# Kernel tuning notes

Measured on AMD Instinct MI355X. Metric: run time of the kernel, lower is better.

Reference implementation:

```python
import jax, jax.numpy as jnp
import numpy as np

PH, CH, Z, H, W, NK = 4, 8, 8, 320, 320, 4096
ITERS, GAMMA, TAU, EPS, RATIO = 3, 0.1, 0.2, 0.01, 0.2
LO, HI = int(Z * RATIO), Z - int(Z * RATIO)  # effective_slice = slice(1, 7)
TWO_PI = 2.0 * np.pi


def to_c(x):
    return jax.lax.complex(x[..., 0], x[..., 1])


def warp(img, flow):
    # MVF motion warp. img: (PH, Z, H, W) complex; flow: (PH, 2, Z, H, W) pixel displacements.
    gy = jnp.clip(jnp.arange(H, dtype=flow.dtype)[:, None] + flow[:, 0], 0.0, H - 1.0)
    gx = jnp.clip(jnp.arange(W, dtype=flow.dtype)[None, :] + flow[:, 1], 0.0, W - 1.0)
    y0 = jnp.floor(gy); x0 = jnp.floor(gx)
    wy = gy - y0; wx = gx - x0
    y0 = y0.astype(jnp.int32); x0 = x0.astype(jnp.int32)
    y1 = jnp.minimum(y0 + 1, H - 1); x1 = jnp.minimum(x0 + 1, W - 1)
    flat = img.reshape(PH, Z, H * W)
    def g(yi, xi):
        return jnp.take_along_axis(flat, (yi * W + xi).reshape(PH, Z, H * W), axis=-1).reshape(PH, Z, H, W)
    return (g(y0, x0) * ((1 - wy) * (1 - wx)) + g(y0, x1) * ((1 - wy) * wx)
            + g(y1, x0) * (wy * (1 - wx)) + g(y1, x1) * (wy * wx))


def nufft(img, traj):
    # Type-2 NUFFT via FFT + bilinear k-space interpolation.
    # img: (PH, CH, Z, H, W) complex; traj: (PH, 2, NK) in [-pi, pi).
    F = jnp.fft.fftshift(jnp.fft.fft2(img), axes=(-2, -1))
    gy = jnp.clip((traj[:, 0] / TWO_PI + 0.5) * H, 0.0, H - 1.0)
    gx = jnp.clip((traj[:, 1] / TWO_PI + 0.5) * W, 0.0, W - 1.0)
    def samp(Fp, gyp, gxp):
        y0 = jnp.floor(gyp); x0 = jnp.floor(gxp)
        wy = gyp - y0; wx = gxp - x0
        y0 = y0.astype(jnp.int32); x0 = x0.astype(jnp.int32)
        y1 = jnp.minimum(y0 + 1, H - 1); x1 = jnp.minimum(x0 + 1, W - 1)
        return (Fp[..., y0, x0] * ((1 - wy) * (1 - wx)) + Fp[..., y0, x1] * ((1 - wy) * wx)
                + Fp[..., y1, x0] * (wy * (1 - wx)) + Fp[..., y1, x1] * (wy * wx))
    return jax.vmap(samp)(F, gy, gx)  # (PH, CH, Z, NK)


def forward_model(x, mvf, csm_c, traj):
    # A = NUFFT * CSM * MVF
    warped = warp(x, mvf)                # (PH, Z, H, W)
    coil = csm_c[None] * warped[:, None]  # (PH, CH, Z, H, W)
    return nufft(coil, traj)             # (PH, CH, Z, NK)


def tv_energy(x):
    # smooth (anisotropic) TV energy; grad_reg = std * d/dx TV(x) = x_eff - regularization(x_eff)
    dy = x[..., 1:, :] - x[..., :-1, :]
    dx = x[..., :, 1:] - x[..., :, :-1]
    return jnp.sum(jnp.sqrt(jnp.abs(dy) ** 2 + 1e-8)) + jnp.sum(jnp.sqrt(jnp.abs(dx) ** 2 + 1e-8))


def setup_inputs():
    key = jax.random.key(0)
    ks = jax.random.split(key, 6)
    kspace_data = 0.1 * jax.random.normal(ks[0], (1, PH, CH, Z, NK, 2), jnp.float32)
    kspace_traj = jax.random.uniform(ks[1], (PH, 2, NK), jnp.float32, -np.pi, np.pi)
    image_init = jax.random.normal(ks[2], (1, PH, Z, H, W, 2), jnp.float32)
    mvf = 2.0 * jax.random.normal(ks[3], (PH, 2, Z, H, W), jnp.float32)
    csm = jax.random.normal(ks[4], (CH, Z, H, W, 2), jnp.float32) / np.sqrt(CH)
    std = jax.random.uniform(ks[5], (1,), jnp.float32, 0.05, 0.15)
    return {"kspace_data": kspace_data, "kspace_traj": kspace_traj, "image_init": image_init,
            "mvf": mvf, "csm": csm, "std": std}


def reference(kspace_data, kspace_traj, image_init, mvf, csm, std):
    y = to_c(kspace_data)[0]                   # (PH, CH, Z, NK)
    x = to_c(jnp.nan_to_num(image_init))[0]     # (PH, Z, H, W)
    csm_c = to_c(csm)                           # (CH, Z, H, W)
    s = std[0]

    def dc_loss(xv):
        est = forward_model(xv, mvf, csm_c, kspace_traj)[:, :, LO:HI]
        det = jax.lax.stop_gradient(jnp.abs(est))
        w = 1.0 / (det / det.max() + EPS)
        d = w * (est - y[:, :, LO:HI])
        # MSE over view_as_real = mean of squared real components
        return 0.5 * (jnp.mean(d.real ** 2) + jnp.mean(d.imag ** 2))

    for _ in range(ITERS):
        g_dc = jax.grad(dc_loss)(x)
        g_tv = s * jax.grad(tv_energy)(x[:, LO:HI])
        g_reg = jnp.zeros_like(x).at[:, LO:HI].set(g_tv)
        x = x - (GAMMA * g_dc + TAU * g_reg)
    return jnp.stack([x.real, x.imag], axis=-1)[None]  # (1, PH, Z, H, W, 2)
```

## Files before the change

kernel.cpp:

```cpp
#include <hip/hip_runtime.h>
#include <math.h>

#define PH   4
#define CHN  8
#define ZT   8
#define ZE   6
#define HG   320
#define WG   320
#define HW2  102400
#define NKP  4096
#define LSTR 321
#define FBCAP 131072u

constexpr float GAMMA_C = 0.1f;
constexpr float TAU_C   = 0.2f;
constexpr float EPS_C   = 0.01f;
constexpr float INV_N   = 1.0f / 786432.0f;
#define TWO_PI_F 6.28318530717958647692f

constexpr float W5R[5] = { 1.f,  0.30901699f, -0.80901699f, -0.80901699f,  0.30901699f};
constexpr float W5I[5] = { 0.f, -0.95105652f, -0.58778525f,  0.58778525f,  0.95105652f};

__device__ __forceinline__ float2 cmul(float2 a, float2 b){
  return make_float2(a.x*b.x - a.y*b.y, a.x*b.y + a.y*b.x);
}
__device__ __forceinline__ void cmac(float2& d, float2 a, float2 b){
  d.x = fmaf(a.x, b.x, fmaf(-a.y, b.y, d.x));
  d.y = fmaf(a.x, b.y, fmaf( a.y, b.x, d.y));
}

__device__ __forceinline__ unsigned pk(float2 v){
  unsigned ua = __float_as_uint(v.x), ub = __float_as_uint(v.y);
  ua = (ua + 0x7FFFu + ((ua >> 16) & 1u)) >> 16;
  ub = (ub + 0x7FFFu + ((ub >> 16) & 1u)) >> 16;
  return ua | (ub << 16);
}
__device__ __forceinline__ float2 upk(unsigned v){
  return make_float2(__uint_as_float(v << 16), __uint_as_float(v & 0xFFFF0000u));
}

__device__ __forceinline__ void corners(float gy, float gx, int& y0, int& x0, int& y1, int& x1,
                                        float& w00, float& w01, float& w10, float& w11){
  float y0f = floorf(gy), x0f = floorf(gx);
  float wy = gy - y0f, wx = gx - x0f;
  y0 = (int)y0f; x0 = (int)x0f;
  y1 = min(y0 + 1, HG - 1); x1 = min(x0 + 1, WG - 1);
  w00 = (1.f - wy) * (1.f - wx);
  w01 = (1.f - wy) * wx;
  w10 = wy * (1.f - wx);
  w11 = wy * wx;
}

__device__ __forceinline__ void traj_to_grid(float ty, float tx, float& gy, float& gx){
  gy = fminf(fmaxf((ty / TWO_PI_F + 0.5f) * 320.f, 0.f), 319.f);
  gx = fminf(fmaxf((tx / TWO_PI_F + 0.5f) * 320.f, 0.f), 319.f);
}

struct FT {
  float2 t1, t2, t3, t4;
  float2 tw0, tw1, tw2, tw3, tw4;
  int br5, lane;
};

__device__ __forceinline__ FT ft_init(){
  FT f; int l = (int)(threadIdx.x & 63); f.lane = l;
  sincosf(-TWO_PI_F * (float)l * (1.0f/320.0f), &f.t1.y, &f.t1.x);
  f.t2 = cmul(f.t1, f.t1); f.t3 = cmul(f.t2, f.t1); f.t4 = cmul(f.t2, f.t2);
  sincosf(-TWO_PI_F * (float)(l & 31) * (1.0f/64.0f), &f.tw0.y, &f.tw0.x);
  sincosf(-TWO_PI_F * (float)(l & 15) * (1.0f/32.0f), &f.tw1.y, &f.tw1.x);
  sincosf(-TWO_PI_F * (float)(l &  7) * (1.0f/16.0f), &f.tw2.y, &f.tw2.x);
  sincosf(-TWO_PI_F * (float)(l &  3) * (1.0f/ 8.0f), &f.tw3.y, &f.tw3.x);
  f.tw4 = (l & 1) ? make_float2(0.f, -1.f) : make_float2(1.f, 0.f);
  int br = ((l&1)<<5) | ((l&2)<<3) | ((l&4)<<1) | ((l&8)>>1) | ((l&16)>>3) | ((l&32)>>5);
  f.br5 = 5 * br;
  return f;
}

template<int H>
__device__ __forceinline__ void bfly(float2& v, float2 tw, int lane){
  float px = __shfl_xor(v.x, H, 64);
  float py = __shfl_xor(v.y, H, 64);
  bool up = (lane & H) != 0;
  float ax = up ? px : v.x, ay = up ? py : v.y;
  float bx = up ? v.x : px, by = up ? v.y : py;
  float dx = ax - bx,  dy = ay - by;
  float mx = fmaf(dx, tw.x, -dy * tw.y);
  float my = fmaf(dx, tw.y,  dy * tw.x);
  v.x = up ? mx : (ax + bx);
  v.y = up ? my : (ay + by);
}

__device__ __forceinline__ void fft320w(const float2 a[5], const FT& f, float2* __restrict__ seg){
  float2 z[5];
  #pragma unroll
  for (int r = 0; r < 5; r++){
    float2 acc = a[0];
    #pragma unroll
    for (int q = 1; q < 5; q++){
      const int j = (q * r) % 5;
      cmac(acc, a[q], make_float2(W5R[j], W5I[j]));
    }
    z[r] = acc;
  }
  z[1] = cmul(z[1], f.t1); z[2] = cmul(z[2], f.t2);
  z[3] = cmul(z[3], f.t3); z[4] = cmul(z[4], f.t4);
  #pragma unroll
  for (int r = 0; r < 5; r++){
    float2 v = z[r];
    bfly<32>(v, f.tw0, f.lane);
    bfly<16>(v, f.tw1, f.lane);
    bfly< 8>(v, f.tw2, f.lane);
    bfly< 4>(v, f.tw3, f.lane);
    bfly< 2>(v, f.tw4, f.lane);
    {
      float px = __shfl_xor(v.x, 1, 64);
      float py = __shfl_xor(v.y, 1, 64);
      bool up = (f.lane & 1) != 0;
      float ax = up ? px : v.x, ay = up ? py : v.y;
      float bx = up ? v.x : px, by = up ? v.y : py;
      v.x = up ? (ax - bx) : (ax + bx);
      v.y = up ? (ay - by) : (ay + by);
    }
    seg[f.br5 + r] = v;
  }
}

__device__ __forceinline__ void fft320w_pk(const float2 a[5], const FT& f, unsigned* __restrict__ seg){
  float2 z[5];
  #pragma unroll
  for (int r = 0; r < 5; r++){
    float2 acc = a[0];
    #pragma unroll
    for (int q = 1; q < 5; q++){
      const int j = (q * r) % 5;
      cmac(acc, a[q], make_float2(W5R[j], W5I[j]));
    }
    z[r] = acc;
  }
  z[1] = cmul(z[1], f.t1); z[2] = cmul(z[2], f.t2);
  z[3] = cmul(z[3], f.t3); z[4] = cmul(z[4], f.t4);
  #pragma unroll
  for (int r = 0; r < 5; r++){
    float2 v = z[r];
    bfly<32>(v, f.tw0, f.lane);
    bfly<16>(v, f.tw1, f.lane);
    bfly< 8>(v, f.tw2, f.lane);
    bfly< 4>(v, f.tw3, f.lane);
    bfly< 2>(v, f.tw4, f.lane);
    {
      float px = __shfl_xor(v.x, 1, 64);
      float py = __shfl_xor(v.y, 1, 64);
      bool up = (f.lane & 1) != 0;
      float ax = up ? px : v.x, ay = up ? py : v.y;
      float bx = up ? v.x : px, by = up ? v.y : py;
      v.x = up ? (ax - bx) : (ax + bx);
      v.y = up ? (ay - by) : (ay + by);
    }
    seg[f.br5 + r] = pk(v);
  }
}

__global__ __launch_bounds__(256) void k_khist(const float* __restrict__ traj, unsigned* __restrict__ xhist){
  int gid = blockIdx.x * 256 + threadIdx.x;
  if (gid >= PH * NKP) return;
  int p = gid >> 12, k = gid & (NKP - 1);
  float gy, gx;
  traj_to_grid(traj[(p * 2 + 0) * NKP + k], traj[(p * 2 + 1) * NKP + k], gy, gx);
  atomicAdd(&xhist[p * WG + (int)floorf(gx)], 1u);
}

__global__ void k_kscan(const unsigned* __restrict__ xhist, unsigned* __restrict__ xcur,
                        unsigned* __restrict__ xbnd){
  int p = threadIdx.x;
  if (p < PH){
    unsigned acc = 0;
    for (int b = 0; b < WG; b++){ xcur[p * WG + b] = acc; xbnd[p * (WG + 1) + b] = acc; acc += xhist[p * WG + b]; }
    xbnd[p * (WG + 1) + WG] = acc;
  }
}

__global__ __launch_bounds__(256) void k_kperm(const float* __restrict__ traj, unsigned* __restrict__ xcur,
                                               float4* __restrict__ permx){
  int gid = blockIdx.x * 256 + threadIdx.x;
  if (gid >= PH * NKP) return;
  int p = gid >> 12, k = gid & (NKP - 1);
  float gy, gx;
  traj_to_grid(traj[(p * 2 + 0) * NKP + k], traj[(p * 2 + 1) * NKP + k], gy, gx);
  unsigned sx = atomicAdd(&xcur[p * WG + (int)floorf(gx)], 1u);
  permx[p * NKP + sx] = make_float4(__uint_as_float((unsigned)k), gy, gx, 0.f);
}

__global__ __launch_bounds__(256) void k_pack_csm(const float2* __restrict__ csm, unsigned* __restrict__ csmb, int n){
  int i = blockIdx.x * 256 + threadIdx.x;
  if (i < n) csmb[i] = pk(csm[i]);
}

__global__ __launch_bounds__(256) void k_init(const float2* __restrict__ img0, float2* __restrict__ x, int n){
  int i = blockIdx.x * 256 + threadIdx.x;
  if (i < n){
    float2 v = img0[i];
    v.x = isnan(v.x) ? 0.f : fminf(fmaxf(v.x, -3.4028235e38f), 3.4028235e38f);
    v.y = isnan(v.y) ? 0.f : fminf(fmaxf(v.y, -3.4028235e38f), 3.4028235e38f);
    x[i] = v;
  }
}

__global__ __launch_bounds__(256) void k_warp_tv(const float2* __restrict__ x, const float* __restrict__ mvf,
                                                 unsigned* __restrict__ warped, unsigned* __restrict__ gtv,
                                                 unsigned int* __restrict__ dmax, unsigned int* __restrict__ fbcnt){
  if (blockIdx.x == 0 && threadIdx.x == 0){ *dmax = 0u; *fbcnt = 0u; }
  int gid = blockIdx.x * 256 + threadIdx.x;
  int hw = gid % HW2;
  int pz = gid / HW2;
  int zz = pz % ZE, p = pz / ZE, z = zz + 1;
  int h = hw / WG, w = hw - h * WG;
  const float* mv = mvf + ((size_t)(p * 2 + 0) * ZT + z) * HW2;
  float fy = mv[hw];
  float fx = mv[(size_t)ZT * HW2 + hw];
  float gy = fminf(fmaxf((float)h + fy, 0.f), 319.f);
  float gx = fminf(fmaxf((float)w + fx, 0.f), 319.f);
  int y0, x0, y1, x1; float w00, w01, w10, w11;
  corners(gy, gx, y0, x0, y1, x1, w00, w01, w10, w11);
  const float2* xs = x + (size_t)(p * ZT + z) * HW2;
  float2 v00 = xs[y0 * WG + x0], v01 = xs[y0 * WG + x1];
  float2 v10 = xs[y1 * WG + x0], v11 = xs[y1 * WG + x1];
  float2 o;
  o.x = v00.x * w00 + v01.x * w01 + v10.x * w10 + v11.x * w11;
  o.y = v00.y * w00 + v01.y * w01 + v10.y * w10 + v11.y * w11;
  warped[gid] = pk(o);
  float2 xc = xs[hw];
  float tre = 0.f, tim = 0.f;
  if (h > 0){
    float2 n = xs[hw - WG];
    float dr = xc.x - n.x, di = xc.y - n.y;
    float r = sqrtf(dr * dr + di * di + 1e-8f);
    tre += dr / r; tim += di / r;
  }
  if (h < HG - 1){
    float2 n = xs[hw + WG];
    float dr = n.x - xc.x, di = n.y - xc.y;
    float r = sqrtf(dr * dr + di * di + 1e-8f);
    tre -= dr / r; tim -= di / r;
  }
  if (w > 0){
    float2 n = xs[hw - 1];
    float dr = xc.x - n.x, di = xc.y - n.y;
    float r = sqrtf(dr * dr + di * di + 1e-8f);
    tre += dr / r; tim += di / r;
  }
  if (w < WG - 1){
    float2 n = xs[hw + 1];
    float dr = n.x - xc.x, di = n.y - xc.y;
    float r = sqrtf(dr * dr + di * di + 1e-8f);
    tre -= dr / r; tim -= di / r;
  }
  gtv[gid] = pk(make_float2(tre, -tim));
}

__global__ __launch_bounds__(512) void k_fft_row_fwd(const unsigned* __restrict__ warped, const unsigned* __restrict__ csmb,
                                                     unsigned* __restrict__ FT_, int p0){
  __shared__ float2 seg[16 * LSTR];
  FT f = ft_init();
  int wid = threadIdx.x >> 6, l = f.lane;
  int hg = blockIdx.x % 20; int sl = blockIdx.x / 20;
  int zz = sl % ZE; int s2 = sl / ZE; int c = s2 % CHN; int pp = s2 / CHN;
  int p = p0 + pp; int z = zz + 1;
  int h0 = hg * 16 + wid * 2;
  const unsigned* wr0 = warped + ((size_t)(p * ZE + zz)) * HW2 + (size_t)h0 * WG;
  const unsigned* cs0 = csmb + ((size_t)(c * ZT + z)) * HW2 + (size_t)h0 * WG;
  float sgn0 = ((h0 + l) & 1) ? -1.f : 1.f;
  float2 a0[5], a1[5];
  #pragma unroll
  for (int q = 0; q < 5; q++){
    float2 v0 = cmul(upk(wr0[64 * q + l]), upk(cs0[64 * q + l]));
    float2 v1 = cmul(upk(wr0[WG + 64 * q + l]), upk(cs0[WG + 64 * q + l]));
    a0[q] = make_float2(v0.x * sgn0, v0.y * sgn0);
    a1[q] = make_float2(-v1.x * sgn0, -v1.y * sgn0);
  }
  fft320w(a0, f, seg + (wid * 2) * LSTR);
  fft320w(a1, f, seg + (wid * 2 + 1) * LSTR);
  __syncthreads();
  unsigned* out = FT_ + (size_t)sl * HW2 + hg * 16;
  for (int i = threadIdx.x; i < 16 * WG; i += 512){
    int w = i >> 4; int hh = i & 15;
    out[(size_t)w * HG + hh] = pk(seg[hh * LSTR + w]);
  }
}

__global__ __launch_bounds__(256) void k_fft_col_sample(const unsigned* __restrict__ FT_, const float4* __restrict__ permx,
                                                        const unsigned* __restrict__ xbnd, float2* __restrict__ est,
                                                        unsigned int* __restrict__ dmax, int p0){
  __shared__ unsigned seg[2][9 * LSTR];
  FT f = ft_init();
  int tid = threadIdx.x; int wid = tid >> 6, l = f.lane;
  int cg = blockIdx.x % 40; int pr = blockIdx.x / 40;
  int sl0 = pr * 2;
  int s2 = sl0 / ZE; int pp = s2 / CHN;
  int p = p0 + pp;
  int cbase = cg * 8;
  const int ncol = (cbase + 8 <= WG - 1) ? 9 : 8;
  const unsigned* Fs0 = FT_ + (size_t)sl0 * HW2 + (size_t)cbase * HG;
  const unsigned* Fs1 = Fs0 + HW2;
  unsigned raw0[3][5], raw1[3][5];
  #pragma unroll
  for (int cc = 0; cc < 3; cc++){
    int col = cc * 4 + wid;
    if (col < 9){
      int colc = min(col, ncol - 1);
      const unsigned* s0 = Fs0 + (size_t)colc * HG;
      const unsigned* s1 = Fs1 + (size_t)colc * HG;
      #pragma unroll
      for (int q = 0; q < 5; q++){ raw0[cc][q] = s0[64 * q + l]; raw1[cc][q] = s1[64 * q + l]; }
    }
  }
  #pragma unroll
  for (int cc = 0; cc < 3; cc++){
    int col = cc * 4 + wid;
    if (col < 9){
      int colc = min(col, ncol - 1);
      float2 a0[5], a1[5];
      #pragma unroll
      for (int q = 0; q < 5; q++){ a0[q] = upk(raw0[cc][q]); a1[q] = upk(raw1[cc][q]); }
      fft320w_pk(a0, f, seg[0] + colc * LSTR);
      fft320w_pk(a1, f, seg[1] + colc * LSTR);
    }
  }
  __syncthreads();
  int lo = (int)xbnd[p * (WG + 1) + cbase];
  int hi = (int)xbnd[p * (WG + 1) + min(cbase + 8, WG)];
  float2* eb0 = est + ((size_t)(p0 * CHN * ZE) + sl0) * NKP;
  float2* eb1 = eb0 + NKP;
  const float4* px = permx + p * NKP;
  float md2 = 0.f;
  for (int j = lo + tid; j < hi; j += 256){
    float4 e4 = px[j];
    int y0, x0, y1, x1; float w00, w01, w10, w11;
    corners(e4.y, e4.z, y0, x0, y1, x1, w00, w01, w10, w11);
    int lc0 = x0 - cbase, lc1 = x1 - cbase;
    {
      float2 v00 = upk(seg[0][lc0 * LSTR + y0]), v01 = upk(seg[0][lc1 * LSTR + y0]);
      float2 v10 = upk(seg[0][lc0 * LSTR + y1]), v11 = upk(seg[0][lc1 * LSTR + y1]);
      float2 e;
      e.x = v00.x * w00 + v01.x * w01 + v10.x * w10 + v11.x * w11;
      e.y = v00.y * w00 + v01.y * w01 + v10.y * w10 + v11.y * w11;
      eb0[j] = e;
      md2 = fmaxf(md2, e.x * e.x + e.y * e.y);
    }
    {
      float2 v00 = upk(seg[1][lc0 * LSTR + y0]), v01 = upk(seg[1][lc1 * LSTR + y0]);
      float2 v10 = upk(seg[1][lc0 * LSTR + y1]), v11 = upk(seg[1][lc1 * LSTR + y1]);
      float2 e;
      e.x = v00.x * w00 + v01.x * w01 + v10.x * w10 + v11.x * w11;
      e.y = v00.y * w00 + v01.y * w01 + v10.y * w10 + v11.y * w11;
      eb1[j] = e;
      md2 = fmaxf(md2, e.x * e.x + e.y * e.y);
    }
  }
  for (int off = 32; off > 0; off >>= 1) md2 = fmaxf(md2, __shfl_down(md2, off, 64));
  if ((tid & 63) == 0 && md2 > 0.f) atomicMax(dmax, __float_as_uint(md2));
}

__global__ __launch_bounds__(256) void k_fft_col_scatter(const float2* __restrict__ est, const float2* __restrict__ kdata,
                                                         const float4* __restrict__ permx,
                                                         const unsigned* __restrict__ xbnd,
                                                         const unsigned int* __restrict__ dmax,
                                                         unsigned* __restrict__ F, int p0){
  __shared__ float2 ld[16 * LSTR];
  FT f = ft_init();
  int tid = threadIdx.x; int wid = tid >> 6, l = f.lane;
  int cg = blockIdx.x % 20; int sl = blockIdx.x / 20;
  int zz = sl % ZE; int s2 = sl / ZE; int c = s2 % CHN; int pp = s2 / CHN;
  int p = p0 + pp; int z = zz + 1;
  for (int i = tid; i < 16 * LSTR; i += 256) ld[i] = make_float2(0.f, 0.f);
  __syncthreads();
  float md = sqrtf(__uint_as_float(*dmax));
  int cbase = cg * 16;
  int lo = (cbase > 0) ? (int)xbnd[p * (WG + 1) + cbase - 1] : 0;
  int hi = (int)xbnd[p * (WG + 1) + min(cbase + 16, WG)];
  const float2* Es = est + ((size_t)(p0 * CHN * ZE) + sl) * NKP;
  const float2* kd = kdata + ((size_t)(p * CHN + c) * ZT + z) * NKP;
  const float4* px = permx + p * NKP;
  for (int j = lo + tid; j < hi; j += 256){
    float4 e4 = px[j];
    int k = (int)__float_as_uint(e4.x);
    int y0, x0, y1, x1; float w00, w01, w10, w11;
    corners(e4.y, e4.z, y0, x0, y1, x1, w00, w01, w10, w11);
    float2 e = Es[j];
    float det = sqrtf(e.x * e.x + e.y * e.y);
    float wv = 1.0f / (det / md + EPS_C);
    float sc = wv * wv * INV_N;
    float2 y = kd[k];
    float2 gv = make_float2(sc * (e.x - y.x), -sc * (e.y - y.y));
    int c0 = x0 - cbase, c1 = x1 - cbase;
    if ((unsigned)c0 < 16u){
      atomicAdd(&ld[c0 * LSTR + y0].x, gv.x * w00); atomicAdd(&ld[c0 * LSTR + y0].y, gv.y * w00);
      atomicAdd(&ld[c0 * LSTR + y1].x, gv.x * w10); atomicAdd(&ld[c0 * LSTR + y1].y, gv.y * w10);
    }
    if ((unsigned)c1 < 16u){
      atomicAdd(&ld[c1 * LSTR + y0].x, gv.x * w01); atomicAdd(&ld[c1 * LSTR + y0].y, gv.y * w01);
      atomicAdd(&ld[c1 * LSTR + y1].x, gv.x * w11); atomicAdd(&ld[c1 * LSTR + y1].y, gv.y * w11);
    }
  }
  __syncthreads();
  #pragma unroll
  for (int cc = 0; cc < 2; cc++){
    float2* base0 = ld + (wid * 4 + cc * 2) * LSTR;
    float2* base1 = base0 + LSTR;
    float2 a0[5], a1[5];
    #pragma unroll
    for (int q = 0; q < 5; q++){ a0[q] = base0[64 * q + l]; a1[q] = base1[64 * q + l]; }
    fft320w(a0, f, base0);
    fft320w(a1, f, base1);
  }
  __syncthreads();
  unsigned* Fs = F + (size_t)sl * HW2 + cbase;
  for (int i = tid; i < 5120; i += 256){ int h = i >> 4, col = i & 15; Fs[h * WG + col] = pk(ld[col * LSTR + h]); }
}

__global__ __launch_bounds__(512) void k_fft_row_bwd(const unsigned* __restrict__ F, const unsigned* __restrict__ csmb,
                                                     unsigned* __restrict__ gwarped, int p0){
  __shared__ float2 seg[2][8 * LSTR];
  FT f = ft_init();
  int tid = threadIdx.x; int c = tid >> 6, l = f.lane;
  int bid = blockIdx.x;
  int h2 = bid % 160; int b2 = bid / 160;
  int zz = b2 % ZE; int pp = b2 / ZE;
  int p = p0 + pp; int z = zz + 1;
  int h0 = h2 * 2;
  const unsigned* Fl = F + ((size_t)((pp * CHN + c) * ZE + zz)) * HW2 + (size_t)h0 * WG;
  float2 a0[5], a1[5];
  #pragma unroll
  for (int q = 0; q < 5; q++){ a0[q] = upk(Fl[64 * q + l]); a1[q] = upk(Fl[WG + 64 * q + l]); }
  fft320w(a0, f, seg[0] + c * LSTR);
  fft320w(a1, f, seg[1] + c * LSTR);
  __syncthreads();
  for (int i = tid; i < 2 * WG; i += 512){
    int hh = i / WG; int w = i - hh * WG;
    int h = h0 + hh;
    float2 acc = make_float2(0.f, 0.f);
    #pragma unroll
    for (int cc = 0; cc < 8; cc++){
      cmac(acc, seg[hh][cc * LSTR + w], upk(csmb[((size_t)(cc * ZT + z)) * HW2 + (size_t)h * WG + w]));
    }
    float sg = ((h + w) & 1) ? -1.f : 1.f;
    gwarped[((size_t)(p * ZE + zz)) * HW2 + (size_t)h * WG + w] = pk(make_float2(acc.x * sg, acc.y * sg));
  }
}

#define TRG 8
#define HAG 8
__global__ __launch_bounds__(512) void k_warpadj_update(const unsigned* __restrict__ gw, const float* __restrict__ mvf,
                                                        const unsigned* __restrict__ gtv, const float* __restrict__ stdp,
                                                        float2* __restrict__ x,
                                                        uint4* __restrict__ fb, unsigned int* __restrict__ fbcnt){
  __shared__ float lt[TRG * WG * 2];
  int tid = threadIdx.x;
  int bid = blockIdx.x;
  int tile = bid % 40; int pz = bid / 40;
  int zz = pz % ZE, p = pz / ZE, z = zz + 1;
  int R = tile * TRG;
  for (int i = tid; i < TRG * WG * 2; i += 512) lt[i] = 0.f;
  __syncthreads();
  const float* mvy = mvf + ((size_t)(p * 2 + 0) * ZT + z) * HW2;
  const float* mvx = mvy + (size_t)ZT * HW2;
  const unsigned* g = gw + (size_t)pz * HW2;
  const size_t xbase = (size_t)(p * ZT + z) * HW2;
  int wlo = max(R - HAG, 0), whi = min(R + TRG + HAG, HG);
  int npx = (whi - wlo) * WG;
  int base0 = wlo * WG;
  int i = tid;
  float fy = 0.f, fx = 0.f; unsigned gvp = 0u;
  if (i < npx){ fy = mvy[base0 + i]; fx = mvx[base0 + i]; gvp = g[base0 + i]; }
  while (i < npx){
    int inx = i + 512;
    float fy2 = 0.f, fx2 = 0.f; unsigned gvp2 = 0u;
    if (inx < npx){ fy2 = mvy[base0 + inx]; fx2 = mvx[base0 + inx]; gvp2 = g[base0 + inx]; }
    int hh = i / WG; int w = i - hh * WG;
    int h = wlo + hh;
    float gy = fminf(fmaxf((float)h + fy, 0.f), 319.f);
    float gx = fminf(fmaxf((float)w + fx, 0.f), 319.f);
    int y0, x0, y1, x1; float w00, w01, w10, w11;
    corners(gy, gx, y0, x0, y1, x1, w00, w01, w10, w11);
    float2 gv = upk(gvp);
    bool owner = (h >= R) && (h < R + TRG);
    #define PROC(Y, XC, WT) { \
      int ry = (Y) - R; \
      if ((unsigned)ry < (unsigned)TRG){ \
        atomicAdd(&lt[(ry * WG + (XC)) * 2 + 0], gv.x * (WT)); \
        atomicAdd(&lt[(ry * WG + (XC)) * 2 + 1], gv.y * (WT)); \
      } else if (owner){ \
        int Ry = (Y) & ~(TRG - 1); \
        if (h < Ry - HAG || h >= Ry + TRG + HAG){ \
          unsigned slot = atomicAdd(fbcnt, 1u); \
          if (slot < FBCAP) fb[slot] = make_uint4((unsigned)(xbase + (size_t)(Y) * WG + (XC)), \
                                                  __float_as_uint(gv.x * (WT)), __float_as_uint(gv.y * (WT)), 0u); \
        } \
      } \
    }
    PROC(y0, x0, w00); PROC(y0, x1, w01); PROC(y1, x0, w10); PROC(y1, x1, w11);
    #undef PROC
    i = inx; fy = fy2; fx = fx2; gvp = gvp2;
  }
  __syncthreads();
  float s = stdp[0];
  const unsigned* gt = gtv + (size_t)pz * HW2;
  for (int i2 = tid; i2 < TRG * WG; i2 += 512){
    int yy = i2 / WG; int w = i2 - yy * WG;
    int hw = (R + yy) * WG + w;
    float2 xv = x[xbase + hw];
    float2 tv = upk(gt[hw]);
    xv.x -= GAMMA_C * lt[i2 * 2 + 0] + TAU_C * s * tv.x;
    xv.y -= GAMMA_C * lt[i2 * 2 + 1] + TAU_C * s * tv.y;
    x[xbase + hw] = xv;
  }
}

__global__ __launch_bounds__(256) void k_fixup(const uint4* __restrict__ fb, const unsigned int* __restrict__ fbcnt,
                                               float2* __restrict__ x){
  unsigned n = *fbcnt; if (n > FBCAP) n = FBCAP;
  for (unsigned i = blockIdx.x * 256 + threadIdx.x; i < n; i += gridDim.x * 256){
    uint4 e = fb[i];
    atomicAdd(&x[e.x].x, -GAMMA_C * __uint_as_float(e.y));
    atomicAdd(&x[e.x].y, -GAMMA_C * __uint_as_float(e.z));
  }
}

extern "C" void kernel_launch(void* const* d_in, const int* in_sizes, int n_in,
                              void* d_out, int out_size, void* d_ws, size_t ws_size,
                              hipStream_t stream) {
  const float2* kdata = (const float2*)d_in[0];
  const float*  traj  = (const float*) d_in[1];
  const float2* img0  = (const float2*)d_in[2];
  const float*  mvf   = (const float*) d_in[3];
  const float2* csm   = (const float2*)d_in[4];
  const float*  stdp  = (const float*) d_in[5];
  float2* x = (float2*)d_out;

  const size_t F_B  = (size_t)CHN * ZE * HW2 * 4;
  const size_t W_B  = (size_t)PH * ZE * HW2 * 4;
  const size_t C_B  = (size_t)CHN * ZT * HW2 * 4;
  const size_t E_B  = (size_t)PH * CHN * ZE * NKP * 8;
  const size_t FB_B = (size_t)FBCAP * 16;
  const size_t P_B  = (size_t)PH * NKP * 16;
  const size_t SORT_B = P_B + 4 * 8192;

  size_t need_big = 4 * F_B + 2 * W_B + C_B + E_B + 512 + FB_B + SORT_B;
  const int NP = (ws_size >= need_big) ? 4 : 1;

  char* cur = (char*)d_ws;
  unsigned* F     = (unsigned*)cur;  cur += (size_t)NP * F_B;
  unsigned* warped= (unsigned*)cur;  cur += W_B;
  float2* est     = (float2*)cur;    cur += E_B;
  unsigned* gtvb  = (unsigned*)cur;  cur += W_B;
  unsigned* csmb  = (unsigned*)cur;  cur += C_B;
  unsigned int* dmax  = (unsigned int*)cur; cur += 128;
  unsigned int* fbcnt = (unsigned int*)cur; cur += 128;
  uint4* fb           = (uint4*)cur;        cur += FB_B;
  float4* permx       = (float4*)cur;       cur += P_B;
  unsigned* xhist     = (unsigned*)cur;     cur += 8192;
  unsigned* xcur      = (unsigned*)cur;     cur += 8192;
  unsigned* xbnd      = (unsigned*)cur;     cur += 8192;

  k_init<<<12800, 256, 0, stream>>>(img0, x, PH * ZT * HW2);
  k_pack_csm<<<25600, 256, 0, stream>>>(csm, csmb, CHN * ZT * HW2);
  hipMemsetAsync(xhist, 0, 8192, stream);
  k_khist<<<64, 256, 0, stream>>>(traj, xhist);
  k_kscan<<<1, 64, 0, stream>>>(xhist, xcur, xbnd);
  k_kperm<<<64, 256, 0, stream>>>(traj, xcur, permx);

  for (int it = 0; it < 3; it++){
    k_warp_tv<<<9600, 256, 0, stream>>>(x, mvf, warped, gtvb, dmax, fbcnt);
    for (int p0 = 0; p0 < PH; p0 += NP){
      k_fft_row_fwd   <<<NP *  960, 512, 0, stream>>>(warped, csmb, F, p0);
      k_fft_col_sample<<<NP *  960, 256, 0, stream>>>(F, permx, xbnd, est, dmax, p0);
    }
    for (int p0 = 0; p0 < PH; p0 += NP){
      k_fft_col_scatter<<<NP *  960, 256, 0, stream>>>(est, kdata, permx, xbnd, dmax, F, p0);
      k_fft_row_bwd    <<<NP *  960, 512, 0, stream>>>(F, csmb, warped, p0);
    }
    k_warpadj_update<<<960, 512, 0, stream>>>(warped, mvf, gtvb, stdp, x, fb, fbcnt);
    k_fixup<<<16, 256, 0, stream>>>(fb, fbcnt, x);
  }
}
```

Measured before the change: 1.478 ms.

## Pre-permute k-space data, pack motion fields to bf16, enlarge warp-adjoint tiles

Adds a one-time kernel that reorders the measured k-space samples into the sorted trajectory order, so the scatter kernel reads them contiguously instead of gathering through the permutation index. Motion-field components are packed once into a single 32-bit pair and read that way by the warp and warp-adjoint kernels, which halves their flow-field loads but stores the flow at reduced precision. The warp-adjoint tile height is doubled and the grid halved, which shrinks the halo overhead per tile at the cost of fewer blocks. Workspace grows by one extra estimate-sized buffer and one motion buffer.

```diff
diff --git a/kernel.cpp b/kernel.cpp
--- a/kernel.cpp
+++ b/kernel.cpp
@@ -190,9 +190,29 @@
   permx[p * NKP + sx] = make_float4(__uint_as_float((unsigned)k), gy, gx, 0.f);
 }
 
+__global__ __launch_bounds__(256) void k_kdperm(const float2* __restrict__ kdata, const float4* __restrict__ permx,
+                                                float2* __restrict__ kdj){
+  int gid = blockIdx.x * 256 + threadIdx.x;
+  int j = gid & (NKP - 1);
+  int t = gid >> 12;
+  int zz = t % ZE; int pc = t / ZE; int p = pc / CHN; int z = zz + 1;
+  int k = (int)__float_as_uint(permx[p * NKP + j].x);
+  kdj[gid] = kdata[((size_t)pc * ZT + z) * NKP + k];
+}
+
 __global__ __launch_bounds__(256) void k_pack_csm(const float2* __restrict__ csm, unsigned* __restrict__ csmb, int n){
   int i = blockIdx.x * 256 + threadIdx.x;
   if (i < n) csmb[i] = pk(csm[i]);
+}
+
+__global__ __launch_bounds__(256) void k_pack_mv(const float* __restrict__ mvf, unsigned* __restrict__ mvp){
+  int gid = blockIdx.x * 256 + threadIdx.x;
+  int hw = gid % HW2;
+  int pz = gid / HW2;
+  int zz = pz % ZE, p = pz / ZE, z = zz + 1;
+  float fy = mvf[((size_t)(p * 2 + 0) * ZT + z) * HW2 + hw];
+  float fx = mvf[((size_t)(p * 2 + 1) * ZT + z) * HW2 + hw];
+  mvp[gid] = pk(make_float2(fy, fx));
 }
 
 __global__ __launch_bounds__(256) void k_init(const float2* __restrict__ img0, float2* __restrict__ x, int n){
@@ -205,7 +225,7 @@
   }
 }
 
-__global__ __launch_bounds__(256) void k_warp_tv(const float2* __restrict__ x, const float* __restrict__ mvf,
+__global__ __launch_bounds__(256) void k_warp_tv(const float2* __restrict__ x, const unsigned* __restrict__ mvp,
                                                  unsigned* __restrict__ warped, unsigned* __restrict__ gtv,
                                                  unsigned int* __restrict__ dmax, unsigned int* __restrict__ fbcnt){
   if (blockIdx.x == 0 && threadIdx.x == 0){ *dmax = 0u; *fbcnt = 0u; }
@@ -214,11 +234,9 @@
   int pz = gid / HW2;
   int zz = pz % ZE, p = pz / ZE, z = zz + 1;
   int h = hw / WG, w = hw - h * WG;
-  const float* mv = mvf + ((size_t)(p * 2 + 0) * ZT + z) * HW2;
-  float fy = mv[hw];
-  float fx = mv[(size_t)ZT * HW2 + hw];
-  float gy = fminf(fmaxf((float)h + fy, 0.f), 319.f);
-  float gx = fminf(fmaxf((float)w + fx, 0.f), 319.f);
+  float2 fv = upk(mvp[gid]);
+  float gy = fminf(fmaxf((float)h + fv.x, 0.f), 319.f);
+  float gx = fminf(fmaxf((float)w + fv.y, 0.f), 319.f);
   int y0, x0, y1, x1; float w00, w01, w10, w11;
   corners(gy, gx, y0, x0, y1, x1, w00, w01, w10, w11);
   const float2* xs = x + (size_t)(p * ZT + z) * HW2;
@@ -360,7 +378,7 @@
   if ((tid & 63) == 0 && md2 > 0.f) atomicMax(dmax, __float_as_uint(md2));
 }
 
-__global__ __launch_bounds__(256) void k_fft_col_scatter(const float2* __restrict__ est, const float2* __restrict__ kdata,
+__global__ __launch_bounds__(256) void k_fft_col_scatter(const float2* __restrict__ est, const float2* __restrict__ kdj,
                                                          const float4* __restrict__ permx,
                                                          const unsigned* __restrict__ xbnd,
                                                          const unsigned int* __restrict__ dmax,
@@ -369,8 +387,8 @@
   FT f = ft_init();
   int tid = threadIdx.x; int wid = tid >> 6, l = f.lane;
   int cg = blockIdx.x % 20; int sl = blockIdx.x / 20;
-  int zz = sl % ZE; int s2 = sl / ZE; int c = s2 % CHN; int pp = s2 / CHN;
-  int p = p0 + pp; int z = zz + 1;
+  int s2 = sl / ZE; int pp = s2 / CHN;
+  int p = p0 + pp;
   for (int i = tid; i < 16 * LSTR; i += 256) ld[i] = make_float2(0.f, 0.f);
   __syncthreads();
   float md = sqrtf(__uint_as_float(*dmax));
@@ -378,18 +396,17 @@
   int lo = (cbase > 0) ? (int)xbnd[p * (WG + 1) + cbase - 1] : 0;
   int hi = (int)xbnd[p * (WG + 1) + min(cbase + 16, WG)];
   const float2* Es = est + ((size_t)(p0 * CHN * ZE) + sl) * NKP;
-  const float2* kd = kdata + ((size_t)(p * CHN + c) * ZT + z) * NKP;
+  const float2* kd = kdj + ((size_t)(p0 * CHN * ZE) + sl) * NKP;
   const float4* px = permx + p * NKP;
   for (int j = lo + tid; j < hi; j += 256){
     float4 e4 = px[j];
-    int k = (int)__float_as_uint(e4.x);
     int y0, x0, y1, x1; float w00, w01, w10, w11;
     corners(e4.y, e4.z, y0, x0, y1, x1, w00, w01, w10, w11);
     float2 e = Es[j];
     float det = sqrtf(e.x * e.x + e.y * e.y);
     float wv = 1.0f / (det / md + EPS_C);
     float sc = wv * wv * INV_N;
-    float2 y = kd[k];
+    float2 y = kd[j];
     float2 gv = make_float2(sc * (e.x - y.x), -sc * (e.y - y.y));
     int c0 = x0 - cbase, c1 = x1 - cbase;
     if ((unsigned)c0 < 16u){
@@ -447,38 +464,38 @@
   }
 }
 
-#define TRG 8
+#define TRG 16
 #define HAG 8
-__global__ __launch_bounds__(512) void k_warpadj_update(const unsigned* __restrict__ gw, const float* __restrict__ mvf,
+__global__ __launch_bounds__(512) void k_warpadj_update(const unsigned* __restrict__ gw, const unsigned* __restrict__ mvp,
                                                         const unsigned* __restrict__ gtv, const float* __restrict__ stdp,
                                                         float2* __restrict__ x,
                                                         uint4* __restrict__ fb, unsigned int* __restrict__ fbcnt){
   __shared__ float lt[TRG * WG * 2];
   int tid = threadIdx.x;
   int bid = blockIdx.x;
-  int tile = bid % 40; int pz = bid / 40;
+  int tile = bid % 20; int pz = bid / 20;
   int zz = pz % ZE, p = pz / ZE, z = zz + 1;
   int R = tile * TRG;
   for (int i = tid; i < TRG * WG * 2; i += 512) lt[i] = 0.f;
   __syncthreads();
-  const float* mvy = mvf + ((size_t)(p * 2 + 0) * ZT + z) * HW2;
-  const float* mvx = mvy + (size_t)ZT * HW2;
+  const unsigned* mvz = mvp + (size_t)pz * HW2;
   const unsigned* g = gw + (size_t)pz * HW2;
   const size_t xbase = (size_t)(p * ZT + z) * HW2;
   int wlo = max(R - HAG, 0), whi = min(R + TRG + HAG, HG);
   int npx = (whi - wlo) * WG;
   int base0 = wlo * WG;
   int i = tid;
-  float fy = 0.f, fx = 0.f; unsigned gvp = 0u;
-  if (i < npx){ fy = mvy[base0 + i]; fx = mvx[base0 + i]; gvp = g[base0 + i]; }
+  unsigned mvv = 0u, gvp = 0u;
+  if (i < npx){ mvv = mvz[base0 + i]; gvp = g[base0 + i]; }
   while (i < npx){
     int inx = i + 512;
-    float fy2 = 0.f, fx2 = 0.f; unsigned gvp2 = 0u;
-    if (inx < npx){ fy2 = mvy[base0 + inx]; fx2 = mvx[base0 + inx]; gvp2 = g[base0 + inx]; }
+    unsigned mvv2 = 0u, gvp2 = 0u;
+    if (inx < npx){ mvv2 = mvz[base0 + inx]; gvp2 = g[base0 + inx]; }
     int hh = i / WG; int w = i - hh * WG;
     int h = wlo + hh;
-    float gy = fminf(fmaxf((float)h + fy, 0.f), 319.f);
-    float gx = fminf(fmaxf((float)w + fx, 0.f), 319.f);
+    float2 fv = upk(mvv);
+    float gy = fminf(fmaxf((float)h + fv.x, 0.f), 319.f);
+    float gx = fminf(fmaxf((float)w + fv.y, 0.f), 319.f);
     int y0, x0, y1, x1; float w00, w01, w10, w11;
     corners(gy, gx, y0, x0, y1, x1, w00, w01, w10, w11);
     float2 gv = upk(gvp);
@@ -499,7 +516,7 @@
     }
     PROC(y0, x0, w00); PROC(y0, x1, w01); PROC(y1, x0, w10); PROC(y1, x1, w11);
     #undef PROC
-    i = inx; fy = fy2; fx = fx2; gvp = gvp2;
+    i = inx; mvv = mvv2; gvp = gvp2;
   }
   __syncthreads();
   float s = stdp[0];
@@ -539,20 +556,23 @@
   const size_t F_B  = (size_t)CHN * ZE * HW2 * 4;
   const size_t W_B  = (size_t)PH * ZE * HW2 * 4;
   const size_t C_B  = (size_t)CHN * ZT * HW2 * 4;
+  const size_t M_B  = (size_t)PH * ZE * HW2 * 4;
   const size_t E_B  = (size_t)PH * CHN * ZE * NKP * 8;
   const size_t FB_B = (size_t)FBCAP * 16;
   const size_t P_B  = (size_t)PH * NKP * 16;
   const size_t SORT_B = P_B + 4 * 8192;
 
-  size_t need_big = 4 * F_B + 2 * W_B + C_B + E_B + 512 + FB_B + SORT_B;
+  size_t need_big = 4 * F_B + 2 * W_B + C_B + M_B + 2 * E_B + 512 + FB_B + SORT_B;
   const int NP = (ws_size >= need_big) ? 4 : 1;
 
   char* cur = (char*)d_ws;
   unsigned* F     = (unsigned*)cur;  cur += (size_t)NP * F_B;
   unsigned* warped= (unsigned*)cur;  cur += W_B;
   float2* est     = (float2*)cur;    cur += E_B;
+  float2* kdj     = (float2*)cur;    cur += E_B;
   unsigned* gtvb  = (unsigned*)cur;  cur += W_B;
   unsigned* csmb  = (unsigned*)cur;  cur += C_B;
+  unsigned* mvp   = (unsigned*)cur;  cur += M_B;
   unsigned int* dmax  = (unsigned int*)cur; cur += 128;
   unsigned int* fbcnt = (unsigned int*)cur; cur += 128;
   uint4* fb           = (uint4*)cur;        cur += FB_B;
@@ -563,22 +583,24 @@
 
   k_init<<<12800, 256, 0, stream>>>(img0, x, PH * ZT * HW2);
   k_pack_csm<<<25600, 256, 0, stream>>>(csm, csmb, CHN * ZT * HW2);
+  k_pack_mv<<<9600, 256, 0, stream>>>(mvf, mvp);
   hipMemsetAsync(xhist, 0, 8192, stream);
   k_khist<<<64, 256, 0, stream>>>(traj, xhist);
   k_kscan<<<1, 64, 0, stream>>>(xhist, xcur, xbnd);
   k_kperm<<<64, 256, 0, stream>>>(traj, xcur, permx);
+  k_kdperm<<<3072, 256, 0, stream>>>(kdata, permx, kdj);
 
   for (int it = 0; it < 3; it++){
-    k_warp_tv<<<9600, 256, 0, stream>>>(x, mvf, warped, gtvb, dmax, fbcnt);
+    k_warp_tv<<<9600, 256, 0, stream>>>(x, mvp, warped, gtvb, dmax, fbcnt);
     for (int p0 = 0; p0 < PH; p0 += NP){
       k_fft_row_fwd   <<<NP *  960, 512, 0, stream>>>(warped, csmb, F, p0);
       k_fft_col_sample<<<NP *  960, 256, 0, stream>>>(F, permx, xbnd, est, dmax, p0);
     }
     for (int p0 = 0; p0 < PH; p0 += NP){
-      k_fft_col_scatter<<<NP *  960, 256, 0, stream>>>(est, kdata, permx, xbnd, dmax, F, p0);
+      k_fft_col_scatter<<<NP *  960, 256, 0, stream>>>(est, kdj, permx, xbnd, dmax, F, p0);
       k_fft_row_bwd    <<<NP *  960, 512, 0, stream>>>(F, csmb, warped, p0);
     }
-    k_warpadj_update<<<960, 512, 0, stream>>>(warped, mvf, gtvb, stdp, x, fb, fbcnt);
+    k_warpadj_update<<<480, 512, 0, stream>>>(warped, mvp, gtvb, stdp, x, fb, fbcnt);
     k_fixup<<<16, 256, 0, stream>>>(fb, fbcnt, x);
   }
 }
```

New measurement: 1.497 ms. About the same (+1.3%).
